# Kernel tuning notes

Hardware: AMD Instinct MI355X
Metric: run time of the kernel (lower is better)

Reference implementation:

```python
import jax, jax.numpy as jnp
import numpy as np

# DCNv4 config (matches init_kwargs)
C = 64; G = 4; GC = C // G          # group channels = 16
KS = 3; KP = KS * KS                # 9 sampling points per group
DIL = 1; OFFSET_SCALE = 1.0
OM_DIM = int(np.ceil(G * KP * 3 / 8) * 8)  # 112 (padded offset+mask dim)
N, H, W = 4, 128, 128


def setup_inputs() -> dict:
    key = jax.random.key(0)
    ks = jax.random.split(key, 5)
    x = jax.random.normal(ks[0], (N, C, H, W), dtype=jnp.float32)
    value_w = jax.random.normal(ks[1], (C, C), dtype=jnp.float32) * (1.0 / np.sqrt(C))
    value_b = jnp.zeros((C,), dtype=jnp.float32)
    # small random offset/mask projection (torch zero-init would be degenerate)
    om_w = jax.random.normal(ks[2], (OM_DIM, C), dtype=jnp.float32) * 0.02
    om_b = jax.random.normal(ks[3], (OM_DIM,), dtype=jnp.float32) * 0.02
    out_w = jax.random.normal(ks[4], (C, C), dtype=jnp.float32) * (1.0 / np.sqrt(C))
    out_b = jnp.zeros((C,), dtype=jnp.float32)
    return {"x": x, "value_w": value_w, "value_b": value_b,
            "om_w": om_w, "om_b": om_b, "out_w": out_w, "out_b": out_b}


def _dcnv4_core(v, off, mask, Hh, Ww):
    # v: (N, L, G, GC)   off: (N, L, G, KP, 2) (x,y)   mask: (N, L, G, KP)
    n, L = v.shape[0], v.shape[1]
    py = (jnp.arange(L) // Ww).astype(jnp.float32)          # (L,)
    px = (jnp.arange(L) % Ww).astype(jnp.float32)
    r = (KS - 1) // 2
    dy, dx = jnp.meshgrid(jnp.arange(-r, r + 1, dtype=jnp.float32) * DIL,
                          jnp.arange(-r, r + 1, dtype=jnp.float32) * DIL,
                          indexing="ij")
    dy = dy.reshape(-1); dx = dx.reshape(-1)                # (KP,)
    # sampling coords: (N, L, G, KP)
    sy = py[None, :, None, None] + dy[None, None, None, :] + off[..., 1] * OFFSET_SCALE
    sx = px[None, :, None, None] + dx[None, None, None, :] + off[..., 0] * OFFSET_SCALE

    y0 = jnp.floor(sy); x0 = jnp.floor(sx)
    wy = sy - y0; wx = sx - x0
    vg = v.transpose(0, 2, 1, 3)                            # (N, G, L, GC)

    def gather(yc, xc, wgt):
        valid = ((yc >= 0) & (yc < Hh) & (xc >= 0) & (xc < Ww)).astype(v.dtype)
        yi = jnp.clip(yc, 0, Hh - 1).astype(jnp.int32)
        xi = jnp.clip(xc, 0, Ww - 1).astype(jnp.int32)
        idx = (yi * Ww + xi).transpose(0, 2, 1, 3).reshape(n, G, L * KP)  # (N,G,L*KP)
        g = jnp.take_along_axis(vg, idx[..., None], axis=2)              # (N,G,L*KP,GC)
        w = (wgt * valid).transpose(0, 2, 1, 3).reshape(n, G, L * KP, 1)
        return g * w

    samp = (gather(y0, x0, (1 - wy) * (1 - wx))
            + gather(y0, x0 + 1, (1 - wy) * wx)
            + gather(y0 + 1, x0, wy * (1 - wx))
            + gather(y0 + 1, x0 + 1, wy * wx))               # (N,G,L*KP,GC)
    samp = samp.reshape(n, G, L, KP, GC)
    m = mask.transpose(0, 2, 1, 3)[..., None]                # (N,G,L,KP,1)
    out = (samp * m).sum(axis=3)                             # (N,G,L,GC)
    return out.transpose(0, 2, 1, 3).reshape(n, L, G * GC)


def reference(x, value_w, value_b, om_w, om_b, out_w, out_b):
    n, c, Hh, Ww = x.shape
    L = Hh * Ww
    inp = x.transpose(0, 2, 3, 1).reshape(n, L, c)           # (N, L, C)
    v = (inp @ value_w.T + value_b).reshape(n, L, G, GC)     # value_proj
    om = inp @ om_w.T + om_b                                 # (N, L, 112)
    om = om[..., :G * KP * 3].reshape(n, L, G, KP * 3)       # per-group [off(2K), mask(K)]
    off = om[..., :2 * KP].reshape(n, L, G, KP, 2)
    mask = om[..., 2 * KP:]                                  # no softmax in DCNv4
    y = _dcnv4_core(v, off, mask, Hh, Ww)                    # (N, L, C)
    y = y @ out_w.T + out_b                                  # output_proj
    return y.reshape(n, Hh, Ww, c).transpose(0, 3, 1, 2)     # (N, C, H, W)
```

## Files before the change

### kernel.cpp

```cpp
#include <hip/hip_runtime.h>

#define NN 4
#define CC 64
#define GG 4
#define GCC 16
#define HH 128
#define WW 128
#define LL (HH*WW)
#define OMS 112
#define WPC 192

__global__ void pack_kernel(const float* __restrict__ value_w, const float* __restrict__ value_b,
                            const float* __restrict__ om_w,    const float* __restrict__ om_b,
                            const float* __restrict__ out_w,
                            float* __restrict__ wpack, float* __restrict__ bpack,
                            float* __restrict__ owt)
{
  const int i = blockIdx.x * 256 + threadIdx.x;
  if (i < 64 * WPC) {
    const int k = i / WPC, c = i % WPC;
    float v = 0.0f;
    if (c < 64) v = value_w[c * 64 + k];
    else if (c < 176) {
      const int s = c - 64;
      if (s % 28 != 27) { const int r = s - s / 28; v = om_w[r * 64 + k]; }
    }
    wpack[i] = v;
  }
  if (i < WPC) {
    float v = 0.0f;
    if (i < 64) v = value_b[i];
    else if (i < 176) {
      const int s = i - 64;
      if (s % 28 != 27) { const int r = s - s / 28; v = om_b[r]; }
    }
    bpack[i] = v;
  }
  if (i < 64 * 64) {
    const int k = i >> 6, c = i & 63;
    owt[i] = out_w[c * 64 + k];
  }
}

__global__ __launch_bounds__(256) void vm_kernel(
    const float* __restrict__ x, const float* __restrict__ wpack,
    const float* __restrict__ bpack,
    float* __restrict__ vws, float* __restrict__ omws)
{
  __shared__ float wlds[64][16];
  const int t    = threadIdx.x;
  const int ch   = blockIdx.y;
  const int col0 = ch << 4;

  {
    const int k = t >> 2, q = t & 3;
    *(float4*)&wlds[k][q * 4] =
        *(const float4*)&wpack[k * WPC + col0 + q * 4];
  }
  float b[16];
  #pragma unroll
  for (int j = 0; j < 16; ++j) b[j] = bpack[col0 + j];
  __syncthreads();

  const int l0  = blockIdx.x << 9;
  const int n   = l0 >> 14;
  const int hw  = (l0 & (LL - 1)) + t;

  float acc0[16], acc1[16];
  #pragma unroll
  for (int j = 0; j < 16; ++j) { acc0[j] = b[j]; acc1[j] = b[j]; }

  const float* xb = x + (size_t)n * CC * LL + hw;
  #pragma unroll 8
  for (int k = 0; k < 64; ++k) {
    const float xv0 = xb[(size_t)k * LL];
    const float xv1 = xb[(size_t)k * LL + 256];
    #pragma unroll
    for (int q = 0; q < 4; ++q) {
      const float4 w = *(const float4*)&wlds[k][q * 4];
      acc0[q*4+0] = fmaf(xv0, w.x, acc0[q*4+0]);
      acc0[q*4+1] = fmaf(xv0, w.y, acc0[q*4+1]);
      acc0[q*4+2] = fmaf(xv0, w.z, acc0[q*4+2]);
      acc0[q*4+3] = fmaf(xv0, w.w, acc0[q*4+3]);
      acc1[q*4+0] = fmaf(xv1, w.x, acc1[q*4+0]);
      acc1[q*4+1] = fmaf(xv1, w.y, acc1[q*4+1]);
      acc1[q*4+2] = fmaf(xv1, w.z, acc1[q*4+2]);
      acc1[q*4+3] = fmaf(xv1, w.w, acc1[q*4+3]);
    }
  }

  float* dst; int col; size_t stride;
  if (ch < 4) { dst = vws  + (size_t)n * LL * 64;  col = col0;      stride = 64;  }
  else        { dst = omws + (size_t)n * LL * OMS; col = col0 - 64; stride = OMS; }
  float* d0 = dst + (size_t)hw * stride + col;
  float* d1 = dst + (size_t)(hw + 256) * stride + col;
  #pragma unroll
  for (int q = 0; q < 4; ++q) {
    *(float4*)&d0[q * 4] = make_float4(acc0[q*4+0], acc0[q*4+1], acc0[q*4+2], acc0[q*4+3]);
    *(float4*)&d1[q * 4] = make_float4(acc1[q*4+0], acc1[q*4+1], acc1[q*4+2], acc1[q*4+3]);
  }
}

__global__ __launch_bounds__(256) void dcn_kernel(
    const float* __restrict__ vws, const float* __restrict__ omws,
    const float* __restrict__ owt, const float* __restrict__ out_b,
    float* __restrict__ out)
{
  __shared__ float s_lds[64][65];
  __shared__ float owlds[64][16*4];
  const int t   = threadIdx.x;
  const int bid = blockIdx.x;
  const int n   = bid >> 8;
  const int p0  = (bid & 255) << 6;

  {
    const float4* src = (const float4*)owt;
    float4*       dstl = (float4*)owlds;
    #pragma unroll
    for (int i = 0; i < 4; ++i) dstl[i * 256 + t] = src[i * 256 + t];
  }

  {
    const int p = t >> 2;
    const int g = t & 3;
    const int l = p0 + p;
    const float pyf = (float)(l >> 7);
    const float pxf = (float)(l & (WW - 1));
    const float* __restrict__ omp_  = omws + ((size_t)n * LL + l) * OMS + g * 28;
    const float* __restrict__ vbase = vws + (size_t)n * LL * CC + g * GCC;

    float buf[28];
    const float4* og4 = (const float4*)omp_;
    #pragma unroll
    for (int i = 0; i < 7; ++i) {
      const float4 vv = og4[i];
      buf[4*i+0] = vv.x; buf[4*i+1] = vv.y; buf[4*i+2] = vv.z; buf[4*i+3] = vv.w;
    }

    float s[16];
    #pragma unroll
    for (int i = 0; i < 16; ++i) s[i] = 0.0f;

    #pragma unroll
    for (int pp = 0; pp < 9; ++pp) {
      const float sy  = pyf + (float)(pp / 3 - 1) + buf[2*pp+1];
      const float sx  = pxf + (float)(pp % 3 - 1) + buf[2*pp+0];
      const float y0f = floorf(sy), x0f = floorf(sx);
      const float wy  = sy - y0f,  wx  = sx - x0f;
      const int   iy  = (int)y0f,  ix  = (int)x0f;
      const float m   = buf[18 + pp];
      const float w00 = (1.0f - wy) * (1.0f - wx) * m;
      const float w01 = (1.0f - wy) * wx * m;
      const float w10 = wy * (1.0f - wx) * m;
      const float w11 = wy * wx * m;
      #pragma unroll
      for (int cor = 0; cor < 4; ++cor) {
        const int   cy = iy + (cor >> 1);
        const int   cx = ix + (cor & 1);
        const float w  = (cor == 0) ? w00 : (cor == 1) ? w01 : (cor == 2) ? w10 : w11;
        if (cy >= 0 && cy < HH && cx >= 0 && cx < WW) {
          const float4* vp4 = (const float4*)(vbase + (size_t)(cy * WW + cx) * CC);
          #pragma unroll
          for (int qq = 0; qq < 4; ++qq) {
            const float4 vv = vp4[qq];
            s[4*qq+0] = fmaf(w, vv.x, s[4*qq+0]);
            s[4*qq+1] = fmaf(w, vv.y, s[4*qq+1]);
            s[4*qq+2] = fmaf(w, vv.z, s[4*qq+2]);
            s[4*qq+3] = fmaf(w, vv.w, s[4*qq+3]);
          }
        }
      }
    }
    #pragma unroll
    for (int j = 0; j < 16; ++j) s_lds[p][g * 16 + j] = s[j];
  }
  __syncthreads();

  {
    const int p  = t & 63;
    const int cq = t >> 6;
    const int l  = p0 + p;
    float y[16];
    #pragma unroll
    for (int j = 0; j < 16; ++j) y[j] = out_b[cq * 16 + j];
    #pragma unroll 8
    for (int k = 0; k < 64; ++k) {
      const float sv = s_lds[p][k];
      #pragma unroll
      for (int q = 0; q < 4; ++q) {
        const float4 w = *(const float4*)&owlds[k][cq * 16 + q * 4];
        y[q*4+0] = fmaf(sv, w.x, y[q*4+0]);
        y[q*4+1] = fmaf(sv, w.y, y[q*4+1]);
        y[q*4+2] = fmaf(sv, w.z, y[q*4+2]);
        y[q*4+3] = fmaf(sv, w.w, y[q*4+3]);
      }
    }
    float* op = out + ((size_t)n * CC) * LL + l;
    #pragma unroll
    for (int j = 0; j < 16; ++j)
      op[(size_t)(cq * 16 + j) * LL] = y[j];
  }
}

extern "C" void kernel_launch(void* const* d_in, const int* in_sizes, int n_in,
                              void* d_out, int out_size, void* d_ws, size_t ws_size,
                              hipStream_t stream) {
  const float* x       = (const float*)d_in[0];
  const float* value_w = (const float*)d_in[1];
  const float* value_b = (const float*)d_in[2];
  const float* om_w    = (const float*)d_in[3];
  const float* om_b    = (const float*)d_in[4];
  const float* out_w   = (const float*)d_in[5];
  const float* out_b   = (const float*)d_in[6];
  float* outp = (float*)d_out;

  float* vws   = (float*)d_ws;
  float* omws  = vws   + (size_t)NN * LL * CC;
  float* wpack = omws  + (size_t)NN * LL * OMS;
  float* bpack = wpack + 64 * WPC;
  float* owt   = bpack + WPC;

  pack_kernel<<<dim3(48), dim3(256), 0, stream>>>(
      value_w, value_b, om_w, om_b, out_w, wpack, bpack, owt);
  vm_kernel<<<dim3(128, 11), dim3(256), 0, stream>>>(
      x, wpack, bpack, vws, omws);
  dcn_kernel<<<dim3(NN * 256), dim3(256), 0, stream>>>(
      vws, omws, owt, out_b, outp);
}
```

Before: 163.0 us.

## Enlarge per-thread tiles in projection kernels and remap DCN blocks to image rows per XCD

The projection kernel now computes four pixels per thread instead of two, so each LDS weight load feeds more FMAs, and launches half as many blocks. The DCN kernel processes a full image row of 128 pixels with 512 threads, uses vectorized LDS stores and loads for the sampled features, and maps block IDs so each XCD handles a contiguous region of one image, which should improve L2 locality for the bilinear gathers. The trade-offs are higher register pressure from the larger accumulators and fewer resident blocks.

Result: no change. 161.0 us (-1.2%).

```diff
diff --git a/kernel.cpp b/kernel.cpp
--- a/kernel.cpp
+++ b/kernel.cpp
@@ -62,70 +62,75 @@
   for (int j = 0; j < 16; ++j) b[j] = bpack[col0 + j];
   __syncthreads();
 
-  const int l0  = blockIdx.x << 9;
-  const int n   = l0 >> 14;
-  const int hw  = (l0 & (LL - 1)) + t;
-
-  float acc0[16], acc1[16];
+  const int l0 = blockIdx.x << 10;
+  const int n  = l0 >> 14;
+  const int hw = (l0 & (LL - 1)) + t;
+
+  float acc[4][16];
   #pragma unroll
-  for (int j = 0; j < 16; ++j) { acc0[j] = b[j]; acc1[j] = b[j]; }
+  for (int pi = 0; pi < 4; ++pi)
+    #pragma unroll
+    for (int j = 0; j < 16; ++j) acc[pi][j] = b[j];
 
   const float* xb = x + (size_t)n * CC * LL + hw;
   #pragma unroll 8
   for (int k = 0; k < 64; ++k) {
-    const float xv0 = xb[(size_t)k * LL];
-    const float xv1 = xb[(size_t)k * LL + 256];
+    float xv[4];
+    #pragma unroll
+    for (int pi = 0; pi < 4; ++pi) xv[pi] = xb[(size_t)k * LL + pi * 256];
     #pragma unroll
     for (int q = 0; q < 4; ++q) {
       const float4 w = *(const float4*)&wlds[k][q * 4];
-      acc0[q*4+0] = fmaf(xv0, w.x, acc0[q*4+0]);
-      acc0[q*4+1] = fmaf(xv0, w.y, acc0[q*4+1]);
-      acc0[q*4+2] = fmaf(xv0, w.z, acc0[q*4+2]);
-      acc0[q*4+3] = fmaf(xv0, w.w, acc0[q*4+3]);
-      acc1[q*4+0] = fmaf(xv1, w.x, acc1[q*4+0]);
-      acc1[q*4+1] = fmaf(xv1, w.y, acc1[q*4+1]);
-      acc1[q*4+2] = fmaf(xv1, w.z, acc1[q*4+2]);
-      acc1[q*4+3] = fmaf(xv1, w.w, acc1[q*4+3]);
-    }
-  }
-
-  float* dst; int col; size_t stride;
+      #pragma unroll
+      for (int pi = 0; pi < 4; ++pi) {
+        acc[pi][q*4+0] = fmaf(xv[pi], w.x, acc[pi][q*4+0]);
+        acc[pi][q*4+1] = fmaf(xv[pi], w.y, acc[pi][q*4+1]);
+        acc[pi][q*4+2] = fmaf(xv[pi], w.z, acc[pi][q*4+2]);
+        acc[pi][q*4+3] = fmaf(xv[pi], w.w, acc[pi][q*4+3]);
+      }
+    }
+  }
+
+  float* dst; int col; int stride;
   if (ch < 4) { dst = vws  + (size_t)n * LL * 64;  col = col0;      stride = 64;  }
   else        { dst = omws + (size_t)n * LL * OMS; col = col0 - 64; stride = OMS; }
-  float* d0 = dst + (size_t)hw * stride + col;
-  float* d1 = dst + (size_t)(hw + 256) * stride + col;
   #pragma unroll
-  for (int q = 0; q < 4; ++q) {
-    *(float4*)&d0[q * 4] = make_float4(acc0[q*4+0], acc0[q*4+1], acc0[q*4+2], acc0[q*4+3]);
-    *(float4*)&d1[q * 4] = make_float4(acc1[q*4+0], acc1[q*4+1], acc1[q*4+2], acc1[q*4+3]);
-  }
-}
-
-__global__ __launch_bounds__(256) void dcn_kernel(
+  for (int pi = 0; pi < 4; ++pi) {
+    float* d = dst + (size_t)(hw + pi * 256) * stride + col;
+    #pragma unroll
+    for (int q = 0; q < 4; ++q)
+      *(float4*)&d[q * 4] =
+          make_float4(acc[pi][q*4+0], acc[pi][q*4+1], acc[pi][q*4+2], acc[pi][q*4+3]);
+  }
+}
+
+__global__ __launch_bounds__(512) void dcn_kernel(
     const float* __restrict__ vws, const float* __restrict__ omws,
     const float* __restrict__ owt, const float* __restrict__ out_b,
     float* __restrict__ out)
 {
-  __shared__ float s_lds[64][65];
-  __shared__ float owlds[64][16*4];
+  __shared__ float s_lds[128][68];
+  __shared__ float owlds[64 * 64];
   const int t   = threadIdx.x;
-  const int bid = blockIdx.x;
-  const int n   = bid >> 8;
-  const int p0  = (bid & 255) << 6;
-
-  {
-    const float4* src = (const float4*)owt;
-    float4*       dstl = (float4*)owlds;
-    #pragma unroll
-    for (int i = 0; i < 4; ++i) dstl[i * 256 + t] = src[i * 256 + t];
+  const int B   = blockIdx.x;
+  const int xcd = B & 7;
+  const int n   = xcd >> 1;
+  const int row = ((xcd & 1) << 6) | (B >> 3);
+  const int l0  = row << 7;
+
+  {
+    const float4* s4 = (const float4*)owt;
+    float4*       d4 = (float4*)owlds;
+    d4[t]       = s4[t];
+    d4[512 + t] = s4[512 + t];
   }
 
   {
     const int p = t >> 2;
     const int g = t & 3;
-    const int l = p0 + p;
-    const float pyf = (float)(l >> 7);
-    const float pxf = (float)(l & (WW - 1));
+    const int l = l0 + p;
+    const float pyf = (float)row;
+    const float pxf = (float)p;
     const float* __restrict__ omp_  = omws + ((size_t)n * LL + l) * OMS + g * 28;
     const float* __restrict__ vbase = vws + (size_t)n * LL * CC + g * GCC;
 
@@ -172,30 +177,37 @@
       }
     }
     #pragma unroll
-    for (int j = 0; j < 16; ++j) s_lds[p][g * 16 + j] = s[j];
+    for (int q = 0; q < 4; ++q)
+      *(float4*)&s_lds[p][g * 16 + q * 4] =
+          make_float4(s[4*q+0], s[4*q+1], s[4*q+2], s[4*q+3]);
   }
   __syncthreads();
 
   {
-    const int p  = t & 63;
-    const int cq = t >> 6;
-    const int l  = p0 + p;
+    const int w  = t >> 6;
+    const int p  = (t & 63) | ((w & 1) << 6);
+    const int cq = w >> 1;
     float y[16];
     #pragma unroll
     for (int j = 0; j < 16; ++j) y[j] = out_b[cq * 16 + j];
-    #pragma unroll 8
-    for (int k = 0; k < 64; ++k) {
-      const float sv = s_lds[p][k];
+    #pragma unroll 4
+    for (int k4 = 0; k4 < 16; ++k4) {
+      const float4 sv = *(const float4*)&s_lds[p][k4 * 4];
       #pragma unroll
-      for (int q = 0; q < 4; ++q) {
-        const float4 w = *(const float4*)&owlds[k][cq * 16 + q * 4];
-        y[q*4+0] = fmaf(sv, w.x, y[q*4+0]);
-        y[q*4+1] = fmaf(sv, w.y, y[q*4+1]);
-        y[q*4+2] = fmaf(sv, w.z, y[q*4+2]);
-        y[q*4+3] = fmaf(sv, w.w, y[q*4+3]);
+      for (int e = 0; e < 4; ++e) {
+        const float se = (e == 0) ? sv.x : (e == 1) ? sv.y : (e == 2) ? sv.z : sv.w;
+        const int   k  = k4 * 4 + e;
+        #pragma unroll
+        for (int q = 0; q < 4; ++q) {
+          const float4 wv = *(const float4*)&owlds[k * 64 + cq * 16 + q * 4];
+          y[q*4+0] = fmaf(se, wv.x, y[q*4+0]);
+          y[q*4+1] = fmaf(se, wv.y, y[q*4+1]);
+          y[q*4+2] = fmaf(se, wv.z, y[q*4+2]);
+          y[q*4+3] = fmaf(se, wv.w, y[q*4+3]);
+        }
       }
     }
-    float* op = out + ((size_t)n * CC) * LL + l;
+    float* op = out + ((size_t)n * CC) * LL + l0 + p;
     #pragma unroll
     for (int j = 0; j < 16; ++j)
       op[(size_t)(cq * 16 + j) * LL] = y[j];
@@ -222,8 +234,8 @@
 
   pack_kernel<<<dim3(48), dim3(256), 0, stream>>>(
       value_w, value_b, om_w, om_b, out_w, wpack, bpack, owt);
-  vm_kernel<<<dim3(128, 11), dim3(256), 0, stream>>>(
+  vm_kernel<<<dim3(64, 11), dim3(256), 0, stream>>>(
       x, wpack, bpack, vws, omws);
-  dcn_kernel<<<dim3(NN * 256), dim3(256), 0, stream>>>(
+  dcn_kernel<<<dim3(512), dim3(512), 0, stream>>>(
       vws, omws, owt, out_b, outp);
 }
```
